# Optimization experiments

Hardware: AMD Instinct MI355X
Metric: run time of the kernel (lower is better)

The kernel has to match this reference:

```python
import jax, jax.numpy as jnp
import numpy as np

N = 50000
E = 800000
D_IN = 128
H = 256
L = 3


def setup_inputs() -> dict:
    key = jax.random.key(0)
    ks = jax.random.split(key, 12)
    x = jax.random.normal(ks[0], (N, D_IN), dtype=jnp.float32)
    edge_index = jax.random.randint(ks[1], (2, E), 0, N, dtype=jnp.int32)
    edge_attr = jax.random.uniform(ks[2], (E, 4), dtype=jnp.float32)
    s_enc = 1.0 / np.sqrt(D_IN)
    s_h = 1.0 / np.sqrt(H)
    W_enc = jax.random.uniform(ks[3], (D_IN, H), minval=-s_enc, maxval=s_enc)
    b_enc = jax.random.uniform(ks[4], (H,), minval=-s_enc, maxval=s_enc)
    W_g = jax.random.uniform(ks[5], (L, H, H), minval=-s_h, maxval=s_h)
    b_g = jax.random.uniform(ks[6], (L, H), minval=-s_h, maxval=s_h)
    W_out = jax.random.uniform(ks[7], (H, H), minval=-s_h, maxval=s_h)
    b_out = jax.random.uniform(ks[8], (H,), minval=-s_h, maxval=s_h)
    return {"x": x, "edge_index": edge_index, "edge_attr": edge_attr,
            "W_enc": W_enc, "b_enc": b_enc, "W_g": W_g, "b_g": b_g,
            "W_out": W_out, "b_out": b_out}


def _gcn_norm(edge_index, n):
    # PyG GCNConv: add self-loops, symmetric normalization D^-1/2 (A+I) D^-1/2
    loops = jnp.arange(n, dtype=edge_index.dtype)
    src = jnp.concatenate([edge_index[0], loops])  # [E+N]
    dst = jnp.concatenate([edge_index[1], loops])  # [E+N]
    deg = jax.ops.segment_sum(jnp.ones_like(dst, dtype=jnp.float32), dst, num_segments=n)
    dinv = jnp.where(deg > 0, jax.lax.rsqrt(deg), 0.0)
    norm = dinv[src] * dinv[dst]  # [E+N]
    return src, dst, norm


def _gcn_conv(h, W, b, src, dst, norm, n):
    m = h @ W                                  # [N,H] transform first
    agg = jax.ops.segment_sum(m[src] * norm[:, None], dst, num_segments=n)
    return agg + b


def reference(x, edge_index, edge_attr, W_enc, b_enc, W_g, b_g, W_out, b_out):
    n = x.shape[0]
    src, dst, norm = _gcn_norm(edge_index, n)
    h = jax.nn.relu(x @ W_enc + b_enc)
    for i in range(W_g.shape[0]):
        h = jax.nn.relu(_gcn_conv(h, W_g[i], b_g[i], src, dst, norm, n))
        # dropout is identity in eval mode
    return h @ W_out + b_out
```

## Files before the change

### kernel.cpp

```cpp
#include <hip/hip_runtime.h>
#include <math.h>

#define N_NODES 50000
#define N_EDGES 800000
#define D_IN    128
#define H_DIM   256
#define L_LAYERS 3
#define SCAN_BLOCKS ((N_NODES + 255) / 256)

typedef _Float16 f16x8 __attribute__((ext_vector_type(8)));
typedef _Float16 f16x4 __attribute__((ext_vector_type(4)));
typedef float    f32x4 __attribute__((ext_vector_type(4)));


__global__ __launch_bounds__(256) void zero_kernel(int* __restrict__ counts,
                                                   int* __restrict__ cursor, int n) {
    int i = blockIdx.x * 256 + threadIdx.x;
    if (i < n) { counts[i] = 0; cursor[i] = 0; }
}

__global__ __launch_bounds__(256) void hist_kernel(const int* __restrict__ dst,
                                                   int* __restrict__ counts, int e_cnt) {
    int e = blockIdx.x * 256 + threadIdx.x;
    if (e < e_cnt) atomicAdd(&counts[dst[e]], 1);
}

__global__ __launch_bounds__(256) void scanA_kernel(const int* __restrict__ counts,
                                                    int* __restrict__ blocksum,
                                                    float* __restrict__ dinv, int n) {
    __shared__ int s[256];
    int t = threadIdx.x;
    int i = blockIdx.x * 256 + t;
    int v = (i < n) ? counts[i] : 0;
    if (i < n) dinv[i] = rsqrtf((float)(v + 1));
    s[t] = v;
    __syncthreads();
#pragma unroll
    for (int d = 128; d > 0; d >>= 1) {
        if (t < d) s[t] += s[t + d];
        __syncthreads();
    }
    if (t == 0) blocksum[blockIdx.x] = s[0];
}

__global__ __launch_bounds__(256) void scanB_kernel(int* __restrict__ blocksum,
                                                    int* __restrict__ offsets,
                                                    int nblocks, int n, int total) {
    __shared__ int s[256];
    int t = threadIdx.x;
    int v = (t < nblocks) ? blocksum[t] : 0;
    s[t] = v;
    __syncthreads();
#pragma unroll
    for (int d = 1; d < 256; d <<= 1) {
        int x = (t >= d) ? s[t - d] : 0;
        __syncthreads();
        s[t] += x;
        __syncthreads();
    }
    if (t < nblocks) blocksum[t] = s[t] - v;
    if (t == 0) offsets[n] = total;
}

__global__ __launch_bounds__(256) void scanC_kernel(const int* __restrict__ counts,
                                                    const int* __restrict__ blocksum,
                                                    int* __restrict__ offsets, int n) {
    __shared__ int s[256];
    int t = threadIdx.x;
    int i = blockIdx.x * 256 + t;
    int v = (i < n) ? counts[i] : 0;
    s[t] = v;
    __syncthreads();
#pragma unroll
    for (int d = 1; d < 256; d <<= 1) {
        int x = (t >= d) ? s[t - d] : 0;
        __syncthreads();
        s[t] += x;
        __syncthreads();
    }
    if (i < n) offsets[i] = blocksum[blockIdx.x] + s[t] - v;
}


__global__ __launch_bounds__(256) void fill_kernel(const int* __restrict__ src,
                                                   const int* __restrict__ dst,
                                                   const int* __restrict__ offsets,
                                                   int* __restrict__ cursor,
                                                   const float* __restrict__ dinv,
                                                   int2* __restrict__ csr, int e_cnt) {
    int e = blockIdx.x * 256 + threadIdx.x;
    if (e < e_cnt) {
        int d = dst[e];
        int pos = offsets[d] + atomicAdd(&cursor[d], 1);
        int s = src[e];
        csr[pos] = make_int2(s, __float_as_int(dinv[s]));
    }
}


__global__ __launch_bounds__(256) void aggregate_kernel(const _Float16* __restrict__ h,
                                                        const int* __restrict__ offsets,
                                                        const int2* __restrict__ csr,
                                                        const float* __restrict__ dinv,
                                                        _Float16* __restrict__ outp, int n) {
    int wave = threadIdx.x >> 6;
    int lane = threadIdx.x & 63;
    int v = blockIdx.x * 4 + wave;
    if (v >= n) return;
    int hi  = lane >> 5;
    int col = (lane & 31) * 8;
    float dv = dinv[v];

    float acc[8];
    f16x8 self = *(const f16x8*)(h + (size_t)v * H_DIM + col);
#pragma unroll
    for (int k = 0; k < 8; ++k) acc[k] = hi ? 0.0f : dv * (float)self[k];

    int e  = offsets[v];
    int e1 = offsets[v + 1];

    for (; e + 15 < e1; e += 16) {
        int2 rec[8]; f16x8 r[8];
#pragma unroll
        for (int j = 0; j < 8; ++j) rec[j] = csr[e + 2 * j + hi];
#pragma unroll
        for (int j = 0; j < 8; ++j) r[j] = *(const f16x8*)(h + (size_t)rec[j].x * H_DIM + col);
#pragma unroll
        for (int j = 0; j < 8; ++j) {
            float w = __int_as_float(rec[j].y);
#pragma unroll
            for (int k = 0; k < 8; ++k) acc[k] += w * (float)r[j][k];
        }
    }
    if (e + 7 < e1) {
        int2 rec[4]; f16x8 r[4];
#pragma unroll
        for (int j = 0; j < 4; ++j) rec[j] = csr[e + 2 * j + hi];
#pragma unroll
        for (int j = 0; j < 4; ++j) r[j] = *(const f16x8*)(h + (size_t)rec[j].x * H_DIM + col);
#pragma unroll
        for (int j = 0; j < 4; ++j) {
            float w = __int_as_float(rec[j].y);
#pragma unroll
            for (int k = 0; k < 8; ++k) acc[k] += w * (float)r[j][k];
        }
        e += 8;
    }
    if (e + 3 < e1) {
        int2 rec[2]; f16x8 r[2];
#pragma unroll
        for (int j = 0; j < 2; ++j) rec[j] = csr[e + 2 * j + hi];
#pragma unroll
        for (int j = 0; j < 2; ++j) r[j] = *(const f16x8*)(h + (size_t)rec[j].x * H_DIM + col);
#pragma unroll
        for (int j = 0; j < 2; ++j) {
            float w = __int_as_float(rec[j].y);
#pragma unroll
            for (int k = 0; k < 8; ++k) acc[k] += w * (float)r[j][k];
        }
        e += 4;
    }
    if (e + 1 < e1) {
        int2 rec = csr[e + hi];
        f16x8 r = *(const f16x8*)(h + (size_t)rec.x * H_DIM + col);
        float w = __int_as_float(rec.y);
#pragma unroll
        for (int k = 0; k < 8; ++k) acc[k] += w * (float)r[k];
        e += 2;
    }
    if (e < e1 && hi == 0) {
        int2 rec = csr[e];
        f16x8 r = *(const f16x8*)(h + (size_t)rec.x * H_DIM + col);
        float w = __int_as_float(rec.y);
#pragma unroll
        for (int k = 0; k < 8; ++k) acc[k] += w * (float)r[k];
    }

#pragma unroll
    for (int k = 0; k < 8; ++k) acc[k] += __shfl_xor(acc[k], 32, 64);

    if (hi == 0) {
        f16x8 o;
#pragma unroll
        for (int k = 0; k < 8; ++k) o[k] = (_Float16)(acc[k] * dv);
        *(f16x8*)(outp + (size_t)v * H_DIM + col) = o;
    }
}


#define WCONV_TOTAL 294912

__global__ __launch_bounds__(256) void wconv_kernel(const float* __restrict__ W_enc,
                                                    const float* __restrict__ W_g,
                                                    const float* __restrict__ W_out,
                                                    _Float16* __restrict__ whi,
                                                    _Float16* __restrict__ wlo) {
    int gid = blockIdx.x * 256 + threadIdx.x;
    if (gid >= WCONV_TOTAL) return;
    const float* src; int base, e;
    if (gid < 32768)       { src = W_enc; base = 0;      e = gid; }
    else if (gid < 229376) { src = W_g;   base = 32768;  e = gid - 32768; }
    else                   { src = W_out; base = 229376; e = gid - 229376; }
    int k = e >> 8;
    int n = e & 255;
    float x = src[e];
    _Float16 hb = (_Float16)x;
    _Float16 lb = (_Float16)(x - (float)hb);
    int dst = base + (k >> 5) * 8192 + (n >> 4) * 512 + ((k & 31) >> 3) * 128
            + (n & 15) * 8 + (k & 7);
    whi[dst] = hb;
    wlo[dst] = lb;
}


template <int KC, int AMODE, int OUT16>
__global__ __launch_bounds__(256, 4) void mfma_gemm(const float* __restrict__ Af,
                                                    const _Float16* __restrict__ A16,
                                                    const _Float16* __restrict__ WhG,
                                                    const _Float16* __restrict__ WlG,
                                                    const float* __restrict__ bias,
                                                    float* __restrict__ Cf,
                                                    _Float16* __restrict__ Ch,
                                                    int n, int relu) {
    constexpr int K   = KC * 32;
    constexpr int PKC = (KC >= 8) ? 4 : KC;
    constexpr int NPH = KC / PKC;
    __shared__ _Float16 Wlds[PKC * 2 * 2048];

    int t = threadIdx.x;
    int w = t >> 6;
    int lane = t & 63;
    int q  = blockIdx.x >> 8;
    int rt = blockIdx.x & 255;
    if (rt * 256 >= n) return;
    int colbase = q * 64;
    int mrow = lane & 15;
    int koct = (lane >> 4) * 8;
    int rbase = rt * 256 + w * 64;

    int rows[4];
#pragma unroll
    for (int mt = 0; mt < 4; ++mt) {
        int r = rbase + mt * 16 + mrow;
        rows[mt] = (r < n) ? r : (n - 1);
    }

    f32x4 acc[4][4];
#pragma unroll
    for (int mt = 0; mt < 4; ++mt)
#pragma unroll
        for (int c = 0; c < 4; ++c)
            acc[mt][c] = (f32x4)(0.0f);

    f16x8 a16p[2][4];
    float4 af0[4], af1[4];
    if (AMODE == 1) {
#pragma unroll
        for (int mt = 0; mt < 4; ++mt) {
            a16p[0][mt] = *(const f16x8*)(A16 + (size_t)rows[mt] * K + koct);
            a16p[1][mt] = *(const f16x8*)(A16 + (size_t)rows[mt] * K + 32 + koct);
        }
    } else {
#pragma unroll
        for (int mt = 0; mt < 4; ++mt) {
            const float* p = Af + (size_t)rows[mt] * K + koct;
            af0[mt] = *(const float4*)p;
            af1[mt] = *(const float4*)(p + 4);
        }
    }

#pragma unroll
    for (int ph = 0; ph < NPH; ++ph) {
        if (ph) __syncthreads();
#pragma unroll
        for (int pk = 0; pk < PKC; ++pk) {
            int kc = ph * PKC + pk;
            __builtin_amdgcn_global_load_lds(
                (const __attribute__((address_space(1))) unsigned int*)(WhG + (size_t)kc * 8192 + q * 2048 + t * 8),
                (__attribute__((address_space(3))) unsigned int*)(&Wlds[(pk * 2 + 0) * 2048 + t * 8]), 16, 0, 0);
            __builtin_amdgcn_global_load_lds(
                (const __attribute__((address_space(1))) unsigned int*)(WlG + (size_t)kc * 8192 + q * 2048 + t * 8),
                (__attribute__((address_space(3))) unsigned int*)(&Wlds[(pk * 2 + 1) * 2048 + t * 8]), 16, 0, 0);
        }
        __syncthreads();

#pragma unroll
        for (int pk = 0; pk < PKC; ++pk) {
            int kc = ph * PKC + pk;
            f16x8 ah[4], al[4];
            if (AMODE == 0) {
#pragma unroll
                for (int mt = 0; mt < 4; ++mt) {
                    float4 c0 = af0[mt], c1 = af1[mt];
                    if (kc + 1 < KC) {
                        const float* p = Af + (size_t)rows[mt] * K + (kc + 1) * 32 + koct;
                        af0[mt] = *(const float4*)p;
                        af1[mt] = *(const float4*)(p + 4);
                    }
                    float xs[8] = {c0.x, c0.y, c0.z, c0.w, c1.x, c1.y, c1.z, c1.w};
                    f16x8 H, L;
#pragma unroll
                    for (int j = 0; j < 8; ++j) {
                        _Float16 hb = (_Float16)xs[j];
                        H[j] = hb;
                        L[j] = (_Float16)(xs[j] - (float)hb);
                    }
                    ah[mt] = H;
                    al[mt] = L;
                }
            }

#pragma unroll
            for (int c = 0; c < 4; ++c) {
                f16x8 bh = *(const f16x8*)&Wlds[(pk * 2 + 0) * 2048 + c * 512 + lane * 8];
                f16x8 bl = *(const f16x8*)&Wlds[(pk * 2 + 1) * 2048 + c * 512 + lane * 8];
#pragma unroll
                for (int mt = 0; mt < 4; ++mt) {
                    if (AMODE == 1) {
                        f16x8 a = a16p[kc & 1][mt];
                        acc[mt][c] = __builtin_amdgcn_mfma_f32_16x16x32_f16(a, bh, acc[mt][c], 0, 0, 0);
                        acc[mt][c] = __builtin_amdgcn_mfma_f32_16x16x32_f16(a, bl, acc[mt][c], 0, 0, 0);
                    } else {
                        acc[mt][c] = __builtin_amdgcn_mfma_f32_16x16x32_f16(ah[mt], bh, acc[mt][c], 0, 0, 0);
                        acc[mt][c] = __builtin_amdgcn_mfma_f32_16x16x32_f16(ah[mt], bl, acc[mt][c], 0, 0, 0);
                        acc[mt][c] = __builtin_amdgcn_mfma_f32_16x16x32_f16(al[mt], bh, acc[mt][c], 0, 0, 0);
                    }
                }
            }

            if (AMODE == 1 && kc + 2 < KC) {
#pragma unroll
                for (int mt = 0; mt < 4; ++mt)
                    a16p[kc & 1][mt] = *(const f16x8*)(A16 + (size_t)rows[mt] * K + (kc + 2) * 32 + koct);
            }
        }
    }

    int colq = lane & 15;
    int rowq = (lane >> 4) * 4;
#pragma unroll
    for (int c = 0; c < 4; ++c) {
        int col = colbase + c * 16 + colq;
        float b = bias[col];
#pragma unroll
        for (int mt = 0; mt < 4; ++mt) {
            int rb = rbase + mt * 16 + rowq;
#pragma unroll
            for (int r = 0; r < 4; ++r) {
                int row = rb + r;
                if (row < n) {
                    float v = acc[mt][c][r] + b;
                    if (relu) v = fmaxf(v, 0.f);
                    if (OUT16) Ch[(size_t)row * H_DIM + col] = (_Float16)v;
                    else       Cf[(size_t)row * H_DIM + col] = v;
                }
            }
        }
    }
}


extern "C" void kernel_launch(void* const* d_in, const int* in_sizes, int n_in,
                              void* d_out, int out_size, void* d_ws, size_t ws_size,
                              hipStream_t stream) {
    const float* x     = (const float*)d_in[0];
    const int*   ei    = (const int*)d_in[1];
    const float* W_enc = (const float*)d_in[3];
    const float* b_enc = (const float*)d_in[4];
    const float* W_g   = (const float*)d_in[5];
    const float* b_g   = (const float*)d_in[6];
    const float* W_out = (const float*)d_in[7];
    const float* b_out = (const float*)d_in[8];
    float* out = (float*)d_out;

    char* ws = (char*)d_ws;
    size_t off = 0;
    auto alloc = [&](size_t bytes) -> void* {
        void* p = ws + off;
        off = (off + bytes + 255) & ~(size_t)255;
        return p;
    };
    int*       counts   = (int*)alloc((size_t)N_NODES * 4);
    int*       offsets  = (int*)alloc((size_t)(N_NODES + 1) * 4);
    int*       cursor   = (int*)alloc((size_t)N_NODES * 4);
    float*     dinv     = (float*)alloc((size_t)N_NODES * 4);
    int*       blocksum = (int*)alloc((size_t)SCAN_BLOCKS * 4);
    int2*      csr      = (int2*)alloc((size_t)N_EDGES * 8);
    _Float16*  h16      = (_Float16*)alloc((size_t)N_NODES * H_DIM * 2);
    _Float16*  agg16    = (_Float16*)alloc((size_t)N_NODES * H_DIM * 2);
    _Float16*  whi      = (_Float16*)alloc((size_t)WCONV_TOTAL * 2);
    _Float16*  wlo      = (_Float16*)alloc((size_t)WCONV_TOTAL * 2);

    const int* src = ei;
    const int* dst = ei + N_EDGES;

    zero_kernel<<<(N_NODES + 255) / 256, 256, 0, stream>>>(counts, cursor, N_NODES);
    hist_kernel<<<(N_EDGES + 255) / 256, 256, 0, stream>>>(dst, counts, N_EDGES);
    scanA_kernel<<<SCAN_BLOCKS, 256, 0, stream>>>(counts, blocksum, dinv, N_NODES);
    scanB_kernel<<<1, 256, 0, stream>>>(blocksum, offsets, SCAN_BLOCKS, N_NODES, N_EDGES);
    scanC_kernel<<<SCAN_BLOCKS, 256, 0, stream>>>(counts, blocksum, offsets, N_NODES);
    fill_kernel<<<(N_EDGES + 255) / 256, 256, 0, stream>>>(src, dst, offsets, cursor, dinv,
                                                           csr, N_EDGES);
    wconv_kernel<<<(WCONV_TOTAL + 255) / 256, 256, 0, stream>>>(W_enc, W_g, W_out, whi, wlo);

    mfma_gemm<4, 0, 1><<<1024, 256, 0, stream>>>(x, (const _Float16*)nullptr,
                                                 whi, wlo, b_enc,
                                                 (float*)nullptr, h16, N_NODES, 1);
    for (int l = 0; l < L_LAYERS; ++l) {
        aggregate_kernel<<<N_NODES / 4, 256, 0, stream>>>(h16, offsets, csr, dinv,
                                                          agg16, N_NODES);
        mfma_gemm<8, 1, 1><<<1024, 256, 0, stream>>>((const float*)nullptr, agg16,
                                                     whi + 32768 + (size_t)l * 65536,
                                                     wlo + 32768 + (size_t)l * 65536,
                                                     b_g + (size_t)l * H_DIM,
                                                     (float*)nullptr, h16, N_NODES, 1);
    }
    mfma_gemm<8, 1, 0><<<1024, 256, 0, stream>>>((const float*)nullptr, h16,
                                                 whi + 229376, wlo + 229376, b_out,
                                                 out, (_Float16*)nullptr, N_NODES, 0);
}
```

Before: 529.3 us.

## Split aggregation across 8 column chunks with 16 edge slots per wave

The aggregate kernel now launches 8 blocks per group of 4 nodes, each covering a 32-column chunk. Within a wave, 16 edge slots each handle 4 column groups, and results are combined with a butterfly shuffle reduction. Before, each wave covered the full 256 columns with 2 edge halves and unrolled up to 8 gathers per lane. The new layout exposes more edge-level parallelism per node, at the cost of 8x more blocks, 8 re-reads of the CSR records and offsets, 32-byte gather segments, and padding lanes that load the node's own row with zero weight.

```diff
diff --git a/kernel.cpp b/kernel.cpp
--- a/kernel.cpp
+++ b/kernel.cpp
@@ -105,81 +105,41 @@
                                                         _Float16* __restrict__ outp, int n) {
     int wave = threadIdx.x >> 6;
     int lane = threadIdx.x & 63;
-    int v = blockIdx.x * 4 + wave;
+    int chunk = blockIdx.x & 7;
+    int v = (blockIdx.x >> 3) * 4 + wave;
     if (v >= n) return;
-    int hi  = lane >> 5;
-    int col = (lane & 31) * 8;
+    int eslot = lane >> 2;
+    int cg    = lane & 3;
+    int col   = chunk * 32 + cg * 8;
     float dv = dinv[v];
 
     float acc[8];
-    f16x8 self = *(const f16x8*)(h + (size_t)v * H_DIM + col);
-#pragma unroll
-    for (int k = 0; k < 8; ++k) acc[k] = hi ? 0.0f : dv * (float)self[k];
-
-    int e  = offsets[v];
+    if (eslot == 0) {
+        f16x8 self = *(const f16x8*)(h + (size_t)v * H_DIM + col);
+#pragma unroll
+        for (int k = 0; k < 8; ++k) acc[k] = dv * (float)self[k];
+    } else {
+#pragma unroll
+        for (int k = 0; k < 8; ++k) acc[k] = 0.0f;
+    }
+
+    int e0 = offsets[v];
     int e1 = offsets[v + 1];
-
-    for (; e + 15 < e1; e += 16) {
-        int2 rec[8]; f16x8 r[8];
-#pragma unroll
-        for (int j = 0; j < 8; ++j) rec[j] = csr[e + 2 * j + hi];
-#pragma unroll
-        for (int j = 0; j < 8; ++j) r[j] = *(const f16x8*)(h + (size_t)rec[j].x * H_DIM + col);
-#pragma unroll
-        for (int j = 0; j < 8; ++j) {
-            float w = __int_as_float(rec[j].y);
-#pragma unroll
-            for (int k = 0; k < 8; ++k) acc[k] += w * (float)r[j][k];
-        }
-    }
-    if (e + 7 < e1) {
-        int2 rec[4]; f16x8 r[4];
-#pragma unroll
-        for (int j = 0; j < 4; ++j) rec[j] = csr[e + 2 * j + hi];
-#pragma unroll
-        for (int j = 0; j < 4; ++j) r[j] = *(const f16x8*)(h + (size_t)rec[j].x * H_DIM + col);
-#pragma unroll
-        for (int j = 0; j < 4; ++j) {
-            float w = __int_as_float(rec[j].y);
-#pragma unroll
-            for (int k = 0; k < 8; ++k) acc[k] += w * (float)r[j][k];
-        }
-        e += 8;
-    }
-    if (e + 3 < e1) {
-        int2 rec[2]; f16x8 r[2];
-#pragma unroll
-        for (int j = 0; j < 2; ++j) rec[j] = csr[e + 2 * j + hi];
-#pragma unroll
-        for (int j = 0; j < 2; ++j) r[j] = *(const f16x8*)(h + (size_t)rec[j].x * H_DIM + col);
-#pragma unroll
-        for (int j = 0; j < 2; ++j) {
-            float w = __int_as_float(rec[j].y);
-#pragma unroll
-            for (int k = 0; k < 8; ++k) acc[k] += w * (float)r[j][k];
-        }
-        e += 4;
-    }
-    if (e + 1 < e1) {
-        int2 rec = csr[e + hi];
+    for (int e = e0; e < e1; e += 16) {
+        int idx = e + eslot;
+        int2 rec = (idx < e1) ? csr[idx] : make_int2(v, 0);
+        float wgt = __int_as_float(rec.y);
         f16x8 r = *(const f16x8*)(h + (size_t)rec.x * H_DIM + col);
-        float w = __int_as_float(rec.y);
-#pragma unroll
-        for (int k = 0; k < 8; ++k) acc[k] += w * (float)r[k];
-        e += 2;
-    }
-    if (e < e1 && hi == 0) {
-        int2 rec = csr[e];
-        f16x8 r = *(const f16x8*)(h + (size_t)rec.x * H_DIM + col);
-        float w = __int_as_float(rec.y);
-#pragma unroll
-        for (int k = 0; k < 8; ++k) acc[k] += w * (float)r[k];
-    }
-
-#pragma unroll
-    for (int k = 0; k < 8; ++k) acc[k] += __shfl_xor(acc[k], 32, 64);
-
-    if (hi == 0) {
+#pragma unroll
+        for (int k = 0; k < 8; ++k) acc[k] += wgt * (float)r[k];
+    }
+
+#pragma unroll
+    for (int m = 4; m <= 32; m <<= 1)
+#pragma unroll
+        for (int k = 0; k < 8; ++k) acc[k] += __shfl_xor(acc[k], m, 64);
+
+    if (eslot == 0) {
         f16x8 o;
 #pragma unroll
         for (int k = 0; k < 8; ++k) o[k] = (_Float16)(acc[k] * dv);
@@ -406,9 +366,10 @@
     mfma_gemm<4, 0, 1><<<1024, 256, 0, stream>>>(x, (const _Float16*)nullptr,
                                                  whi, wlo, b_enc,
                                                  (float*)nullptr, h16, N_NODES, 1);
+    int agg_grid = 8 * ((N_NODES + 3) / 4);
     for (int l = 0; l < L_LAYERS; ++l) {
-        aggregate_kernel<<<N_NODES / 4, 256, 0, stream>>>(h16, offsets, csr, dinv,
-                                                          agg16, N_NODES);
+        aggregate_kernel<<<agg_grid, 256, 0, stream>>>(h16, offsets, csr, dinv,
+                                                       agg16, N_NODES);
         mfma_gemm<8, 1, 1><<<1024, 256, 0, stream>>>((const float*)nullptr, agg16,
                                                      whi + 32768 + (size_t)l * 65536,
                                                      wlo + 32768 + (size_t)l * 65536,
```

Result: slower. 777.8 us (+47.0%).
